# Kernel tuning notes

Hardware: AMD Instinct MI355X
Metric: run time of the kernel (lower is better)

The kernel has to match this reference:

```python
import jax, jax.numpy as jnp
import numpy as np

TEMPERATURE = 0.8
TOP_P = 0.9
NEG_INF = float('-inf')


def _top_k_filter(logits, k):
    # keep only the top-k logits per row; mask the rest to -inf.
    # torch.topk + scatter mask == threshold at the k-th largest value (ties measure-zero for float logits)
    kth = jax.lax.top_k(logits, k)[0][..., -1:]  # [B, 1]
    return jnp.where(logits < kth, NEG_INF, logits)


def _top_p_filter(logits, p):
    # nucleus filtering: sort desc, cumulative softmax mass, drop tail past p (always keep the top token)
    B, V = logits.shape
    order = jnp.argsort(-logits, axis=-1)                       # [B, V] descending order
    sorted_logits = jnp.take_along_axis(logits, order, axis=-1)
    cdf = jnp.cumsum(jax.nn.softmax(sorted_logits, axis=-1), axis=-1)
    remove_sorted = cdf > p
    remove_sorted = jnp.roll(remove_sorted, 1, axis=-1).at[..., 0].set(False)  # shift so first token crossing p is kept
    rows = jnp.arange(B)[:, None]
    remove = jnp.zeros((B, V), dtype=bool).at[rows, order].set(remove_sorted)  # scatter back to original positions
    return jnp.where(remove, NEG_INF, logits)


def _sample_multinomial(probs, key):
    # inverse-CDF sampling: idx = #{cumsum <= r}
    r = jax.random.uniform(key, (probs.shape[0], 1), dtype=probs.dtype)
    cdf = jnp.cumsum(probs, axis=-1)
    return jnp.sum(cdf <= r, axis=-1, keepdims=True)  # [B, 1] int


def setup_inputs() -> dict:
    key = jax.random.key(0)
    logits = jax.random.normal(key, (256, 50257), dtype=jnp.float32) * 4.0
    return {"logits": logits, "top_k": 50}


def reference(logits, top_k):
    logits = logits / TEMPERATURE
    logits = _top_k_filter(logits, top_k)
    logits = _top_p_filter(logits, TOP_P)
    probs = jax.nn.softmax(logits, axis=-1)
    next_ids = _sample_multinomial(probs, jax.random.fold_in(jax.random.key(0), 1))
    return next_ids
```

## Files before the change

### kernel.cpp

```cpp
#include <hip/hip_runtime.h>
#include <stdint.h>


#define BLOCK  1024
#define CAPN   2048
#define SLOTS  (CAPN / 64)
#define WCAP   256
#define TOPP   0.9f
#define TOPT_F 8.0f
#define OK8    0xC1000000u

__device__ __forceinline__ unsigned orderKey(float x) {
  unsigned u = __float_as_uint(x);
  return (u & 0x80000000u) ? ~u : (u | 0x80000000u);
}

__device__ __forceinline__ void threefry2x32(unsigned k0, unsigned k1,
                                             unsigned x0, unsigned x1,
                                             unsigned &o0, unsigned &o1) {
  unsigned k2 = k0 ^ k1 ^ 0x1BD11BDAu;
  x0 += k0; x1 += k1;
#define TFR(rr) { x0 += x1; x1 = (x1 << (rr)) | (x1 >> (32 - (rr))); x1 ^= x0; }
  TFR(13) TFR(15) TFR(26) TFR(6)
  x0 += k1; x1 += k2 + 1u;
  TFR(17) TFR(29) TFR(16) TFR(24)
  x0 += k2; x1 += k0 + 2u;
  TFR(13) TFR(15) TFR(26) TFR(6)
  x0 += k0; x1 += k1 + 3u;
  TFR(17) TFR(29) TFR(16) TFR(24)
  x0 += k1; x1 += k2 + 4u;
  TFR(13) TFR(15) TFR(26) TFR(6)
  x0 += k2; x1 += k0 + 5u;
#undef TFR
  o0 = x0; o1 = x1;
}

__global__ __launch_bounds__(BLOCK) void k_all(
    const float* __restrict__ logits, const int* __restrict__ topk_ptr,
    int* __restrict__ out, int V) {
  __shared__ float    bufv[CAPN];
  __shared__ int      bufi[CAPN];
  __shared__ float    wv[WCAP];
  __shared__ int      wi[WCAP];
  __shared__ float    sv[WCAP];
  __shared__ int      si[WCAP];
  __shared__ float    evl[WCAP];
  __shared__ short    ordl[WCAP];
  __shared__ unsigned lcnt, wcnt;
  __shared__ int      s_slow, s_tot;
  __shared__ unsigned s_thr;
  __shared__ int      redc[BLOCK / 64];

  const int tid = threadIdx.x, lane = tid & 63, wid = tid >> 6;
  const int row = blockIdx.x;
  const float* __restrict__ rp = logits + (size_t)row * (size_t)V;
  const float4* __restrict__ rp4 = (const float4*)rp;
  const int V4 = V >> 2;

  int k = topk_ptr[0];
  if (k < 1) k = 1;
  if (k > V) k = V;

  if (tid == 0) { lcnt = 0u; wcnt = 0u; }
  __syncthreads();

#define PUSH(v_, idx_) do {                                             \
    bool q_ = (v_) >= TOPT_F;                                           \
    unsigned long long m_ = __ballot(q_);                               \
    if (q_) {                                                           \
      int ldr_ = __ffsll((unsigned long long)m_) - 1;                   \
      unsigned base_;                                                   \
      if (lane == ldr_) base_ = atomicAdd(&lcnt, (unsigned)__popcll(m_)); \
      base_ = __shfl(base_, ldr_);                                      \
      unsigned p_ = base_ + (unsigned)__popcll(m_ & ((1ull << lane) - 1ull)); \
      if (p_ < CAPN) { bufv[p_] = (v_); bufi[p_] = (idx_); }            \
    } } while (0)

  const int V4m = V4 & ~(4 * BLOCK - 1);
  for (int base = 0; base < V4m; base += 4 * BLOCK) {
    const int i0 = base + tid;
    float4 a = rp4[i0];
    float4 b = rp4[i0 + BLOCK];
    float4 c = rp4[i0 + 2 * BLOCK];
    float4 d = rp4[i0 + 3 * BLOCK];
    PUSH(a.x, (i0 << 2));                PUSH(a.y, (i0 << 2) + 1);
    PUSH(a.z, (i0 << 2) + 2);            PUSH(a.w, (i0 << 2) + 3);
    PUSH(b.x, ((i0 + BLOCK) << 2));      PUSH(b.y, ((i0 + BLOCK) << 2) + 1);
    PUSH(b.z, ((i0 + BLOCK) << 2) + 2);  PUSH(b.w, ((i0 + BLOCK) << 2) + 3);
    PUSH(c.x, ((i0 + 2 * BLOCK) << 2));     PUSH(c.y, ((i0 + 2 * BLOCK) << 2) + 1);
    PUSH(c.z, ((i0 + 2 * BLOCK) << 2) + 2); PUSH(c.w, ((i0 + 2 * BLOCK) << 2) + 3);
    PUSH(d.x, ((i0 + 3 * BLOCK) << 2));     PUSH(d.y, ((i0 + 3 * BLOCK) << 2) + 1);
    PUSH(d.z, ((i0 + 3 * BLOCK) << 2) + 2); PUSH(d.w, ((i0 + 3 * BLOCK) << 2) + 3);
  }
  for (int i = V4m + tid; i < V4; i += BLOCK) {
    float4 a = rp4[i];
    PUSH(a.x, (i << 2));     PUSH(a.y, (i << 2) + 1);
    PUSH(a.z, (i << 2) + 2); PUSH(a.w, (i << 2) + 3);
  }
  for (int i = (V4 << 2) + tid; i < V; i += BLOCK) PUSH(rp[i], i);
#undef PUSH
  __syncthreads();

  if (wid == 0) {
    const int n = ((int)lcnt > CAPN) ? CAPN : (int)lcnt;
    unsigned key[SLOTS];
#pragma unroll
    for (int s = 0; s < SLOTS; ++s) {
      int i = lane + (s << 6);
      key[s] = (i < n) ? orderKey(bufv[i]) : 0u;
    }
    bool ok = (lcnt <= (unsigned)CAPN) && (n >= k);
    unsigned kraw = 0u;
    if (ok) {
      unsigned lo = 1u, hi = 0xFFFFFFFFu;
      while (lo < hi) {
        unsigned mid = lo + ((hi - lo + 1u) >> 1);
        int c = 0;
#pragma unroll
        for (int s = 0; s < SLOTS; ++s)
          if ((s << 6) < n) c += __popcll(__ballot(key[s] >= mid));
        if (c >= k) lo = mid; else hi = mid - 1u;
      }
      kraw = lo;
      ok = (kraw >= OK8 + 4u);
    }
    if (lane == 0) { s_slow = ok ? 0 : 1; s_thr = ok ? (kraw - 4u) : 0u; }
  }
  __syncthreads();

  if (s_slow) {
    unsigned lo = 1u, hi = 0xFFFFFFFFu;
    while (lo < hi) {
      unsigned mid = lo + ((hi - lo + 1u) >> 1);
      int c = 0;
      for (int i = tid; i < V; i += BLOCK) c += (orderKey(rp[i]) >= mid);
      for (int o = 32; o; o >>= 1) c += __shfl_down(c, o);
      if (lane == 0) redc[wid] = c;
      __syncthreads();
      if (tid == 0) {
        int t = 0;
        for (int w = 0; w < BLOCK / 64; ++w) t += redc[w];
        s_tot = t;
      }
      __syncthreads();
      if (s_tot >= k) lo = mid; else hi = mid - 1u;
      __syncthreads();
    }
    if (tid == 0) { lcnt = 0u; s_thr = (lo >= 5u) ? lo - 4u : 1u; }
    __syncthreads();
    const unsigned thr = s_thr;
    for (int i = tid; i < V; i += BLOCK) {
      float x = rp[i];
      if (orderKey(x) >= thr) {
        unsigned p = atomicAdd(&lcnt, 1u);
        if (p < CAPN) { bufv[p] = x; bufi[p] = i; }
      }
    }
    __syncthreads();
  }

  if (wid != 0) return;

  const int n = ((int)lcnt > CAPN) ? CAPN : (int)lcnt;
  const unsigned thr = s_thr;

  for (int i = lane; i < n; i += 64) {
    float x = bufv[i];
    if (orderKey(x) >= thr) {
      unsigned p = atomicAdd(&wcnt, 1u);
      if (p < WCAP) { wv[p] = x / 0.8f; wi[p] = bufi[i]; }
    }
  }
  int m = (int)wcnt;
  if (m > WCAP) m = WCAP;
  if (m == 0) { if (lane == 0) out[row] = V; return; }

  unsigned skey[WCAP / 64];
#pragma unroll
  for (int s = 0; s < WCAP / 64; ++s) {
    int i = lane + (s << 6);
    skey[s] = (i < m) ? orderKey(wv[i]) : 0u;
  }
  const int kk = (k < m) ? k : m;
  unsigned lo = 1u, hi = 0xFFFFFFFFu;
  while (lo < hi) {
    unsigned mid = lo + ((hi - lo + 1u) >> 1);
    int c = 0;
#pragma unroll
    for (int s = 0; s < WCAP / 64; ++s)
      c += __popcll(__ballot(skey[s] >= mid));
    if (c >= kk) lo = mid; else hi = mid - 1u;
  }
  const unsigned kvs = lo;
  int ns = 0;
#pragma unroll
  for (int s = 0; s < WCAP / 64; ++s)
    ns += __popcll(__ballot(skey[s] >= kvs));

  for (int i = lane; i < m; i += 64) {
    float v = wv[i];
    int   id = wi[i];
    int   rk = 0;
    for (int j = 0; j < m; ++j) {
      float vj = wv[j];
      rk += (vj > v) || (vj == v && wi[j] < id);
    }
    sv[rk] = v;
    si[rk] = id;
  }

  unsigned tk0, tk1, o0, o1;
  threefry2x32(0u, 0u, 0u, 1u, tk0, tk1);
  threefry2x32(tk0, tk1, 0u, (unsigned)row, o0, o1);
  unsigned bits = o0 ^ o1;
  float r0 = __uint_as_float((bits >> 9) | 0x3F800000u) - 1.0f;
  const float rr = (r0 < 0.f) ? 0.f : r0;

  if (ns <= 64) {
    float myv  = (lane < ns) ? sv[lane] : 0.f;
    int   myid = (lane < ns) ? si[lane] : 0x7FFFFFFF;
    const float mx = __shfl(myv, 0);
    float mye = (lane < ns) ? expf(myv - mx) : 0.f;

    float S = 0.f;
    for (int i = 0; i < ns; ++i) S += __shfl(mye, i);
    float c = 0.f;
    int K = ns;
    for (int i = 0; i < ns; ++i) {
      if (i > 0 && c > TOPP) { K = i; break; }
      c += __shfl(mye, i) / S;
    }
    float S2 = 0.f;
    for (int i = 0; i < K; ++i) S2 += __shfl(mye, i);

    int rk = 0;
    for (int j = 0; j < K; ++j) {
      int idj = __shfl(myid, j);
      rk += (idj < myid);
    }
    float c2 = 0.f;
    int ans = V;
    for (int t = 0; t < K; ++t) {
      unsigned long long mm = __ballot((lane < K) && (rk == t));
      int src = __ffsll((unsigned long long)mm) - 1;
      c2 += __shfl(mye, src) / S2;
      if (c2 > rr) { ans = __shfl(myid, src); break; }
    }
    if (lane == 0) out[row] = ans;
    return;
  }

  for (int i = lane; i < ns; i += 64) evl[i] = expf(sv[i] - sv[0]);
  if (lane == 0) {
    float S = 0.f;
    for (int i = 0; i < ns; ++i) S += evl[i];
    float c = 0.f;
    int K = ns;
    for (int i = 0; i < ns; ++i) {
      if (i > 0 && c > TOPP) { K = i; break; }
      c += evl[i] / S;
    }
    float S2 = 0.f;
    for (int i = 0; i < K; ++i) S2 += evl[i];
    for (int i = 0; i < K; ++i) {
      int id = si[i], rk2 = 0;
      for (int j = 0; j < K; ++j) rk2 += (si[j] < id);
      ordl[rk2] = (short)i;
    }
    float c2 = 0.f;
    int ans = V;
    for (int t = 0; t < K; ++t) {
      int i = ordl[t];
      c2 += evl[i] / S2;
      if (c2 > rr) { ans = si[i]; break; }
    }
    out[row] = ans;
  }
}

extern "C" void kernel_launch(void* const* d_in, const int* in_sizes, int n_in,
                              void* d_out, int out_size, void* d_ws, size_t ws_size,
                              hipStream_t stream) {
  const float* logits = (const float*)d_in[0];
  const int*   topk   = (const int*)d_in[1];
  int*         out    = (int*)d_out;
  const int B = out_size;
  const int V = in_sizes[0] / B;
  (void)d_ws; (void)ws_size; (void)n_in;
  hipLaunchKernelGGL(k_all, dim3(B), dim3(BLOCK), 0, stream,
                     logits, topk, out, V);
}
```

Before: 120.9 us.

## Split row scan across chunked blocks and select the top-k threshold with a histogram

Replaces the single 1024-thread-per-row kernel with two kernels. The first spreads each row over 8 blocks of 256 threads that write candidates above a fixed cutoff to per-chunk segments in global workspace. The second gathers those segments, finds the top-k threshold bucket with a 256-bin histogram instead of a per-lane binary search, and computes the rank cut with a block-wide rank sort. The aim is more parallelism on the memory-bound scan (2048 blocks instead of 256) and a cheaper threshold search, at the cost of a second launch and a global round-trip for the candidates.

```diff
diff --git a/kernel.cpp b/kernel.cpp
--- a/kernel.cpp
+++ b/kernel.cpp
@@ -2,13 +2,15 @@
 #include <stdint.h>
 
 
-#define BLOCK  1024
-#define CAPN   2048
-#define SLOTS  (CAPN / 64)
-#define WCAP   256
-#define TOPP   0.9f
-#define TOPT_F 8.0f
-#define OK8    0xC1000000u
+#define S_CHUNKS 8
+#define PB       256
+#define SEG      256
+#define TB       256
+#define CAPN     2048
+#define WCAP     256
+#define TOPP     0.9f
+#define TOPT_F   8.0f
+#define OK8      0xC1000000u
 
 __device__ __forceinline__ unsigned orderKey(float x) {
   unsigned u = __float_as_uint(x);
@@ -35,169 +37,187 @@
   o0 = x0; o1 = x1;
 }
 
-__global__ __launch_bounds__(BLOCK) void k_all(
-    const float* __restrict__ logits, const int* __restrict__ topk_ptr,
+__global__ __launch_bounds__(PB) void k_pass1(
+    const float* __restrict__ logits, int* __restrict__ scnt,
+    uint2* __restrict__ seg, int V) {
+  __shared__ unsigned lcnt;
+
+  const int row = blockIdx.y, chunk = blockIdx.x, tid = threadIdx.x;
+  const float* __restrict__ rp = logits + (size_t)row * (size_t)V;
+  const float4* __restrict__ rp4 = (const float4*)rp;
+  const int V4 = V >> 2;
+  const int beg = (int)((long long)chunk * V4 / S_CHUNKS);
+  const int end = (int)((long long)(chunk + 1) * V4 / S_CHUNKS);
+  const bool last = (chunk == S_CHUNKS - 1);
+  const int rembeg = V4 << 2;
+  const int sb = row * S_CHUNKS + chunk;
+  uint2* __restrict__ op = seg + (size_t)sb * SEG;
+
+  if (tid == 0) lcnt = 0u;
+  __syncthreads();
+
+#define EMIT(xv, xi) do { float _x = (xv);                               \
+    if (_x >= TOPT_F) { unsigned _p = atomicAdd(&lcnt, 1u);              \
+      if (_p < SEG) op[_p] = make_uint2(__float_as_uint(_x), (unsigned)(xi)); \
+    } } while (0)
+
+  for (int i = beg + tid; i < end; i += PB) {
+    float4 v = rp4[i];
+    EMIT(v.x, (i << 2));     EMIT(v.y, (i << 2) + 1);
+    EMIT(v.z, (i << 2) + 2); EMIT(v.w, (i << 2) + 3);
+  }
+  if (last)
+    for (int i = rembeg + tid; i < V; i += PB) EMIT(rp[i], i);
+#undef EMIT
+  __syncthreads();
+  if (tid == 0) scnt[sb] = (lcnt > (unsigned)SEG) ? -1 : (int)lcnt;
+}
+
+__global__ __launch_bounds__(TB) void k_tail(
+    const float* __restrict__ logits, const int* __restrict__ scnt,
+    const uint2* __restrict__ seg, const int* __restrict__ topk_ptr,
     int* __restrict__ out, int V) {
-  __shared__ float    bufv[CAPN];
-  __shared__ int      bufi[CAPN];
+  __shared__ float    candv[CAPN];
+  __shared__ int      candi[CAPN];
+  __shared__ unsigned hist2[TB];
   __shared__ float    wv[WCAP];
   __shared__ int      wi[WCAP];
   __shared__ float    sv[WCAP];
   __shared__ int      si[WCAP];
   __shared__ float    evl[WCAP];
   __shared__ short    ordl[WCAP];
-  __shared__ unsigned lcnt, wcnt;
-  __shared__ int      s_slow, s_tot;
-  __shared__ unsigned s_thr;
-  __shared__ int      redc[BLOCK / 64];
+  __shared__ int      s_off[S_CHUNKS + 1];
+  __shared__ int      s_c[S_CHUNKS];
+  __shared__ unsigned s_wc, s_thr;
+  __shared__ int      s_n, s_bstar, s_mode, s_ns;
 
   const int tid = threadIdx.x, lane = tid & 63, wid = tid >> 6;
   const int row = blockIdx.x;
   const float* __restrict__ rp = logits + (size_t)row * (size_t)V;
-  const float4* __restrict__ rp4 = (const float4*)rp;
-  const int V4 = V >> 2;
-
   int k = topk_ptr[0];
   if (k < 1) k = 1;
   if (k > V) k = V;
 
-  if (tid == 0) { lcnt = 0u; wcnt = 0u; }
-  __syncthreads();
-
-#define PUSH(v_, idx_) do {                                             \
-    bool q_ = (v_) >= TOPT_F;                                           \
-    unsigned long long m_ = __ballot(q_);                               \
-    if (q_) {                                                           \
-      int ldr_ = __ffsll((unsigned long long)m_) - 1;                   \
-      unsigned base_;                                                   \
-      if (lane == ldr_) base_ = atomicAdd(&lcnt, (unsigned)__popcll(m_)); \
-      base_ = __shfl(base_, ldr_);                                      \
-      unsigned p_ = base_ + (unsigned)__popcll(m_ & ((1ull << lane) - 1ull)); \
-      if (p_ < CAPN) { bufv[p_] = (v_); bufi[p_] = (idx_); }            \
-    } } while (0)
-
-  const int V4m = V4 & ~(4 * BLOCK - 1);
-  for (int base = 0; base < V4m; base += 4 * BLOCK) {
-    const int i0 = base + tid;
-    float4 a = rp4[i0];
-    float4 b = rp4[i0 + BLOCK];
-    float4 c = rp4[i0 + 2 * BLOCK];
-    float4 d = rp4[i0 + 3 * BLOCK];
-    PUSH(a.x, (i0 << 2));                PUSH(a.y, (i0 << 2) + 1);
-    PUSH(a.z, (i0 << 2) + 2);            PUSH(a.w, (i0 << 2) + 3);
-    PUSH(b.x, ((i0 + BLOCK) << 2));      PUSH(b.y, ((i0 + BLOCK) << 2) + 1);
-    PUSH(b.z, ((i0 + BLOCK) << 2) + 2);  PUSH(b.w, ((i0 + BLOCK) << 2) + 3);
-    PUSH(c.x, ((i0 + 2 * BLOCK) << 2));     PUSH(c.y, ((i0 + 2 * BLOCK) << 2) + 1);
-    PUSH(c.z, ((i0 + 2 * BLOCK) << 2) + 2); PUSH(c.w, ((i0 + 2 * BLOCK) << 2) + 3);
-    PUSH(d.x, ((i0 + 3 * BLOCK) << 2));     PUSH(d.y, ((i0 + 3 * BLOCK) << 2) + 1);
-    PUSH(d.z, ((i0 + 3 * BLOCK) << 2) + 2); PUSH(d.w, ((i0 + 3 * BLOCK) << 2) + 3);
-  }
-  for (int i = V4m + tid; i < V4; i += BLOCK) {
-    float4 a = rp4[i];
-    PUSH(a.x, (i << 2));     PUSH(a.y, (i << 2) + 1);
-    PUSH(a.z, (i << 2) + 2); PUSH(a.w, (i << 2) + 3);
-  }
-  for (int i = (V4 << 2) + tid; i < V; i += BLOCK) PUSH(rp[i], i);
-#undef PUSH
-  __syncthreads();
-
-  if (wid == 0) {
-    const int n = ((int)lcnt > CAPN) ? CAPN : (int)lcnt;
-    unsigned key[SLOTS];
-#pragma unroll
-    for (int s = 0; s < SLOTS; ++s) {
-      int i = lane + (s << 6);
-      key[s] = (i < n) ? orderKey(bufv[i]) : 0u;
-    }
-    bool ok = (lcnt <= (unsigned)CAPN) && (n >= k);
-    unsigned kraw = 0u;
-    if (ok) {
-      unsigned lo = 1u, hi = 0xFFFFFFFFu;
-      while (lo < hi) {
-        unsigned mid = lo + ((hi - lo + 1u) >> 1);
-        int c = 0;
-#pragma unroll
-        for (int s = 0; s < SLOTS; ++s)
-          if ((s << 6) < n) c += __popcll(__ballot(key[s] >= mid));
-        if (c >= k) lo = mid; else hi = mid - 1u;
-      }
-      kraw = lo;
-      ok = (kraw >= OK8 + 4u);
-    }
-    if (lane == 0) { s_slow = ok ? 0 : 1; s_thr = ok ? (kraw - 4u) : 0u; }
-  }
-  __syncthreads();
-
-  if (s_slow) {
+  if (tid < S_CHUNKS) s_c[tid] = scnt[row * S_CHUNKS + tid];
+  if (tid == 0) s_wc = 0u;
+  __syncthreads();
+  if (tid == 0) {
+    int off = 0, bad = 0;
+    for (int c = 0; c < S_CHUNKS; ++c) {
+      int cc = s_c[c];
+      if (cc < 0) { bad = 1; cc = 0; }
+      s_off[c] = off;
+      off += cc;
+    }
+    int n = bad ? -1 : off;
+    if (n > CAPN) n = -1;
+    s_off[S_CHUNKS] = n;
+    s_mode = (n < k) ? 1 : 0;
+  }
+  __syncthreads();
+  int n = s_off[S_CHUNKS];
+
+  if (s_mode == 0) {
+    for (int c = 0; c < S_CHUNKS; ++c) {
+      const int o = s_off[c];
+      const int cn = ((c + 1 < S_CHUNKS) ? s_off[c + 1] : n) - o;
+      const uint2* __restrict__ gp = seg + (size_t)(row * S_CHUNKS + c) * SEG;
+      for (int i = tid; i < cn; i += TB) {
+        uint2 u = gp[i];
+        candv[o + i] = __uint_as_float(u.x);
+        candi[o + i] = (int)u.y;
+      }
+    }
+    hist2[tid] = 0u;
+    __syncthreads();
+    for (int i = tid; i < n; i += TB) {
+      unsigned b = (orderKey(candv[i]) - OK8) >> 16;
+      if (b > 255u) b = 255u;
+      atomicAdd(&hist2[b], 1u);
+    }
+    __syncthreads();
+    if (wid == 0) {
+      unsigned h0 = hist2[4 * lane],     h1 = hist2[4 * lane + 1];
+      unsigned h2 = hist2[4 * lane + 2], h3 = hist2[4 * lane + 3];
+      int suf = (int)(h0 + h1 + h2 + h3);
+      for (int d = 1; d < 64; d <<= 1) {
+        int t = __shfl_down(suf, d);
+        if (lane + d < 64) suf += t;
+      }
+      int sufn = (lane < 63) ? __shfl_down(suf, 1) : 0;
+      unsigned long long mk = __ballot(suf >= k);
+      int Ls = (int)__popcll(mk) - 1;
+      if (lane == Ls) {
+        int cum = sufn, bs;
+        if (cum + (int)h3 >= k) bs = 4 * Ls + 3;
+        else { cum += (int)h3;
+          if (cum + (int)h2 >= k) bs = 4 * Ls + 2;
+          else { cum += (int)h2;
+            bs = (cum + (int)h1 >= k) ? 4 * Ls + 1 : 4 * Ls; } }
+        s_bstar = bs;
+      }
+    }
+    __syncthreads();
+    if (tid == 0) {
+      int b = s_bstar;
+      if (b >= 1) s_thr = OK8 + ((unsigned)b << 16) - 4u;
+      else        s_mode = 1;
+    }
+    __syncthreads();
+  }
+
+  if (s_mode == 1) {
     unsigned lo = 1u, hi = 0xFFFFFFFFu;
     while (lo < hi) {
       unsigned mid = lo + ((hi - lo + 1u) >> 1);
       int c = 0;
-      for (int i = tid; i < V; i += BLOCK) c += (orderKey(rp[i]) >= mid);
-      for (int o = 32; o; o >>= 1) c += __shfl_down(c, o);
-      if (lane == 0) redc[wid] = c;
+      for (int i = tid; i < V; i += TB) c += (orderKey(rp[i]) >= mid);
+      hist2[tid] = (unsigned)c;
       __syncthreads();
-      if (tid == 0) {
-        int t = 0;
-        for (int w = 0; w < BLOCK / 64; ++w) t += redc[w];
-        s_tot = t;
-      }
+      for (int st = TB / 2; st; st >>= 1) {
+        if (tid < st) hist2[tid] += hist2[tid + st];
+        __syncthreads();
+      }
+      unsigned tot = hist2[0];
       __syncthreads();
-      if (s_tot >= k) lo = mid; else hi = mid - 1u;
-      __syncthreads();
-    }
-    if (tid == 0) { lcnt = 0u; s_thr = (lo >= 5u) ? lo - 4u : 1u; }
+      if ((int)tot >= k) lo = mid; else hi = mid - 1u;
+    }
+    if (tid == 0) { s_thr = (lo >= 5u) ? lo - 4u : 1u; s_wc = 0u; }
     __syncthreads();
     const unsigned thr = s_thr;
-    for (int i = tid; i < V; i += BLOCK) {
+    for (int i = tid; i < V; i += TB) {
       float x = rp[i];
       if (orderKey(x) >= thr) {
-        unsigned p = atomicAdd(&lcnt, 1u);
-        if (p < CAPN) { bufv[p] = x; bufi[p] = i; }
-      }
-    }
-    __syncthreads();
-  }
-
-  if (wid != 0) return;
-
-  const int n = ((int)lcnt > CAPN) ? CAPN : (int)lcnt;
-  const unsigned thr = s_thr;
-
-  for (int i = lane; i < n; i += 64) {
-    float x = bufv[i];
-    if (orderKey(x) >= thr) {
-      unsigned p = atomicAdd(&wcnt, 1u);
-      if (p < WCAP) { wv[p] = x / 0.8f; wi[p] = bufi[i]; }
-    }
-  }
-  int m = (int)wcnt;
+        unsigned p = atomicAdd(&s_wc, 1u);
+        if (p < CAPN) { candv[p] = x; candi[p] = i; }
+      }
+    }
+    __syncthreads();
+    if (tid == 0) {
+      int nn = (int)s_wc;
+      s_n = (nn > CAPN) ? CAPN : nn;
+      s_wc = 0u;
+    }
+    __syncthreads();
+    n = s_n;
+  }
+
+  {
+    const unsigned thr = s_thr;
+    for (int i = tid; i < n; i += TB) {
+      float x = candv[i];
+      if (orderKey(x) >= thr) {
+        unsigned p = atomicAdd(&s_wc, 1u);
+        if (p < WCAP) { wv[p] = x / 0.8f; wi[p] = candi[i]; }
+      }
+    }
+  }
+  __syncthreads();
+  int m = (int)s_wc;
   if (m > WCAP) m = WCAP;
-  if (m == 0) { if (lane == 0) out[row] = V; return; }
-
-  unsigned skey[WCAP / 64];
-#pragma unroll
-  for (int s = 0; s < WCAP / 64; ++s) {
-    int i = lane + (s << 6);
-    skey[s] = (i < m) ? orderKey(wv[i]) : 0u;
-  }
-  const int kk = (k < m) ? k : m;
-  unsigned lo = 1u, hi = 0xFFFFFFFFu;
-  while (lo < hi) {
-    unsigned mid = lo + ((hi - lo + 1u) >> 1);
-    int c = 0;
-#pragma unroll
-    for (int s = 0; s < WCAP / 64; ++s)
-      c += __popcll(__ballot(skey[s] >= mid));
-    if (c >= kk) lo = mid; else hi = mid - 1u;
-  }
-  const unsigned kvs = lo;
-  int ns = 0;
-#pragma unroll
-  for (int s = 0; s < WCAP / 64; ++s)
-    ns += __popcll(__ballot(skey[s] >= kvs));
-
-  for (int i = lane; i < m; i += 64) {
+  if (m == 0) { if (tid == 0) out[row] = V; return; }
+
+  for (int i = tid; i < m; i += TB) {
     float v = wv[i];
     int   id = wi[i];
     int   rk = 0;
@@ -208,6 +228,19 @@
     sv[rk] = v;
     si[rk] = id;
   }
+  __syncthreads();
+
+  if (tid == 0) {
+    const int kk = (k < m) ? k : m;
+    int ns = kk;
+    float kv = sv[kk - 1];
+    while (ns < m && sv[ns] == kv) ++ns;
+    s_ns = ns;
+  }
+  __syncthreads();
+  const int ns = s_ns;
+
+  if (wid != 0) return;
 
   unsigned tk0, tk1, o0, o1;
   threefry2x32(0u, 0u, 0u, 1u, tk0, tk1);
@@ -286,7 +319,13 @@
   int*         out    = (int*)d_out;
   const int B = out_size;
   const int V = in_sizes[0] / B;
-  (void)d_ws; (void)ws_size; (void)n_in;
-  hipLaunchKernelGGL(k_all, dim3(B), dim3(BLOCK), 0, stream,
-                     logits, topk, out, V);
-}
+
+  char* ws = (char*)d_ws;
+  int*   scnt = (int*)ws;
+  uint2* seg  = (uint2*)(ws + (size_t)B * S_CHUNKS * 4);
+
+  hipLaunchKernelGGL(k_pass1, dim3(S_CHUNKS, B), dim3(PB), 0, stream,
+                     logits, scnt, seg, V);
+  hipLaunchKernelGGL(k_tail, dim3(B), dim3(TB), 0, stream,
+                     logits, scnt, seg, topk, out, V);
+}
```

After: 108.4 us. 10.3% less time.
